# Kernel optimization log

Hardware: AMD Instinct MI355X
Metric: run time of the kernel (lower is better)

## Reference

```python
import jax, jax.numpy as jnp
import numpy as np

N_NODES = 100000
N_EDGES = 500000
N_GRAPHS = 128
HID = 128          # Config.hidden_dim
KEY_EMB = HID // 4 # 32
IN_DIM = 16
FEAT_DIM = IN_DIM - 1  # key feature removed
OUT_DIM = 2
MSG_IN = 2 * HID + 1   # 257


def setup_inputs() -> dict:
    key = jax.random.key(0)
    ks = jax.random.split(key, 24)
    p = lambda k, shp: (jax.random.normal(k, shp, dtype=jnp.float32) * 0.02)
    inp = {
        "x": jax.random.normal(ks[0], (N_NODES, IN_DIM), dtype=jnp.float32),
        "W_enc": p(ks[1], (1, KEY_EMB)), "b_enc": jnp.zeros((KEY_EMB,), jnp.float32),
        "W0": p(ks[2], (FEAT_DIM + KEY_EMB, HID)), "b0": jnp.zeros((HID,), jnp.float32),
        "W1a": p(ks[3], (MSG_IN, HID)), "b1a": jnp.zeros((HID,), jnp.float32),
        "W1b": p(ks[4], (HID, HID)), "b1b": jnp.zeros((HID,), jnp.float32),
        "W2a": p(ks[5], (MSG_IN, HID)), "b2a": jnp.zeros((HID,), jnp.float32),
        "W2b": p(ks[6], (HID, HID)), "b2b": jnp.zeros((HID,), jnp.float32),
        "Wf1": p(ks[7], (4 * HID, HID)), "bf1": jnp.zeros((HID,), jnp.float32),
        "Wf2": p(ks[8], (HID, OUT_DIM)), "bf2": jnp.zeros((OUT_DIM,), jnp.float32),
        "edge_src1": jax.random.randint(ks[9], (N_EDGES,), 0, N_NODES),
        "edge_dst1": jax.random.randint(ks[10], (N_EDGES,), 0, N_NODES),
        "edge_src2": jax.random.randint(ks[11], (N_EDGES,), 0, N_NODES),
        "edge_dst2": jax.random.randint(ks[12], (N_EDGES,), 0, N_NODES),
        "batch": jnp.sort(jax.random.randint(ks[13], (N_NODES,), 0, N_GRAPHS)),
    }
    return inp


def _leaky_relu(v):
    return jnp.where(v > 0, v, 0.1 * v)


def _edge_conv(h, key_feat, src, dst, Wa, ba, Wb, bb):
    # message: [x_j - x_i, x_i, key_j - key_i] -> Linear -> LeakyReLU(0.1) -> Linear
    h_i = h[dst]                      # [E, HID] target
    h_j = h[src]                      # [E, HID] source
    m = jnp.concatenate([h_j - h_i, h_i, key_feat[src] - key_feat[dst]], axis=-1)  # [E, 257]
    m = _leaky_relu(jnp.dot(m, Wa) + ba)
    m = jnp.dot(m, Wb) + bb
    agg = jax.ops.segment_max(m, dst, num_segments=N_NODES)
    agg = jnp.where(jnp.isfinite(agg), agg, 0.0)  # nodes with no in-edges -> 0 (PyG scatter-max fill)
    return agg + h  # residual


def reference(x, W_enc, b_enc, W0, b0, W1a, b1a, W1b, b1b, W2a, b2a, W2b, b2b,
              Wf1, bf1, Wf2, bf2, edge_src1, edge_dst1, edge_src2, edge_dst2, batch):
    key_feat = x[:, 0:1]              # key_feature_idx = 0
    features = x[:, 1:]               # [N, FEAT_DIM]
    key_emb = jnp.dot(key_feat, W_enc) + b_enc  # [N, 32]
    h = jax.nn.relu(jnp.dot(jnp.concatenate([features, key_emb], axis=-1), W0) + b0)  # dropout: eval mode

    x1 = jax.nn.relu(_edge_conv(h, key_feat, edge_src1, edge_dst1, W1a, b1a, W1b, b1b))
    x2 = jax.nn.relu(_edge_conv(x1, key_feat, edge_src2, edge_dst2, W2a, b2a, W2b, b2b))

    cat = jnp.concatenate([x1, x2], axis=1)  # [N, 256]
    max_pool = jax.ops.segment_max(cat, batch, num_segments=N_GRAPHS)
    max_pool = jnp.where(jnp.isfinite(max_pool), max_pool, 0.0)
    counts = jax.ops.segment_sum(jnp.ones((N_NODES,), jnp.float32), batch, num_segments=N_GRAPHS)
    mean_pool = jax.ops.segment_sum(cat, batch, num_segments=N_GRAPHS) / jnp.maximum(counts, 1.0)[:, None]

    pooled = jnp.concatenate([max_pool, mean_pool], axis=1)  # [G, 512]
    out = jnp.dot(jax.nn.relu(jnp.dot(pooled, Wf1) + bf1), Wf2) + bf2
    return jax.nn.log_softmax(out, axis=1)
```

## Files before the change

kernel.cpp:

```cpp
#include <hip/hip_runtime.h>
#include <cstdint>

#define N_NODES 100000
#define N_EDGES 500000
#define N_GRAPHS 128
#define HID 128
#define SCANH_B ((N_NODES + 255) / 256)
#define E256_G ((N_EDGES + 255) / 256)
#define MM_G ((N_NODES + 127) / 128)
#define AH_G ((N_NODES + 511) / 512)
#define BH_G ((N_EDGES + 511) / 512)
#define EDGE_G ((N_EDGES + 63) / 64)

typedef __attribute__((ext_vector_type(8))) short short8;
typedef __attribute__((ext_vector_type(4))) float f32x4;

__device__ __forceinline__ unsigned encf(float f) {
    unsigned u = __float_as_uint(f);
    return (u & 0x80000000u) ? ~u : (u | 0x80000000u);
}
__device__ __forceinline__ float decf(unsigned e) {
    unsigned u = (e & 0x80000000u) ? (e & 0x7FFFFFFFu) : ~e;
    return __uint_as_float(u);
}
__device__ __forceinline__ unsigned cvt_pk_bf16(float lo, float hi) {
    unsigned r;
    asm("v_cvt_pk_bf16_f32 %0, %1, %2" : "=v"(r) : "v"(lo), "v"(hi));
    return r;
}
__device__ __forceinline__ ushort bf16r(float f) {
    unsigned u = __float_as_uint(f);
    return (ushort)((u + 0x7fffu + ((u >> 16) & 1u)) >> 16);
}
__device__ __forceinline__ float bf2f(ushort h) {
    return __uint_as_float((unsigned)h << 16);
}

__global__ __launch_bounds__(256) void prep_hist_kernel(const float* __restrict__ W1b,
                                                        const float* __restrict__ W2b,
                                                        const float* __restrict__ W1a,
                                                        const float* __restrict__ W2a,
                                                        const float* __restrict__ W_enc,
                                                        const float* __restrict__ b_enc,
                                                        const float* __restrict__ W0,
                                                        const float* __restrict__ b0,
                                                        ushort* __restrict__ WT,
                                                        float* __restrict__ wkey,
                                                        float* __restrict__ bias0,
                                                        float* __restrict__ pooled,
                                                        const int* __restrict__ dst1,
                                                        int* __restrict__ cnt,
                                                        int* __restrict__ seq) {
    int blk = blockIdx.x;
    int tid = threadIdx.x;
    if (blk < E256_G) {
        int e = blk * 256 + tid;
        if (e < N_EDGES) seq[e] = atomicAdd(&cnt[dst1[e]], 1);
        return;
    }
    int b2 = blk - E256_G;
    if (b2 < 384) {
        int m = b2 >> 6;
        int i = (b2 & 63) * 256 + tid;
        int n = i >> 7, k = i & 127;
        int src = k * HID + n;
        float v;
        switch (m) {
            case 0: v = W1b[src]; break;
            case 1: v = W2b[src]; break;
            case 2: v = W1a[src]; break;
            case 3: v = W1a[HID * HID + src] - W1a[src]; break;
            case 4: v = W2a[src]; break;
            default: v = W2a[HID * HID + src] - W2a[src]; break;
        }
        WT[m * HID * HID + i] = bf16r(v);
        return;
    }
    if (b2 == 384) {
        if (tid < HID) {
            float wk = 0.f, bk = b0[tid];
            for (int k = 0; k < 32; ++k) {
                float w = W0[(15 + k) * HID + tid];
                wk += W_enc[k] * w;
                bk += b_enc[k] * w;
            }
            wkey[tid] = wk;
            bias0[tid] = bk;
        }
        return;
    }
    pooled[(b2 - 385) * 256 + tid] = 0.f;
}

__global__ __launch_bounds__(256) void scan_half_kernel(const int* __restrict__ cnt,
                                                        int* __restrict__ cursor,
                                                        int* __restrict__ partials) {
    __shared__ int tmp[256];
    int tid = threadIdx.x;
    int gid = blockIdx.x * 256 + tid;
    int v = (gid < N_NODES) ? cnt[gid] : 0;
    tmp[tid] = v;
    __syncthreads();
#pragma unroll
    for (int off = 1; off < 256; off <<= 1) {
        int t = (tid >= off) ? tmp[tid - off] : 0;
        __syncthreads();
        tmp[tid] += t;
        __syncthreads();
    }
    if (gid < N_NODES) cursor[gid] = tmp[tid] - v;
    if (tid == 255) partials[blockIdx.x] = tmp[255];
}

__global__ __launch_bounds__(512) void scan2_half_kernel(int* __restrict__ partials) {
    __shared__ int tmp[512];
    int tid = threadIdx.x;
    int v = (tid < SCANH_B) ? partials[tid] : 0;
    tmp[tid] = v;
    __syncthreads();
#pragma unroll
    for (int off = 1; off < 512; off <<= 1) {
        int t = (tid >= off) ? tmp[tid - off] : 0;
        __syncthreads();
        tmp[tid] += t;
        __syncthreads();
    }
    if (tid < SCANH_B) partials[tid] = tmp[tid] - v;
}

__global__ __launch_bounds__(512, 4) void build_mm_kernel(const float* __restrict__ x,
                                                          const float* __restrict__ W0,
                                                          const float* __restrict__ wkey,
                                                          const float* __restrict__ bias0,
                                                          ushort* __restrict__ h,
                                                          float* __restrict__ xkey,
                                                          const ushort* __restrict__ WuT,
                                                          const ushort* __restrict__ WvT,
                                                          const float* __restrict__ bv,
                                                          ushort* __restrict__ outu,
                                                          ushort* __restrict__ outv,
                                                          const int* __restrict__ src1,
                                                          const int* __restrict__ dst1,
                                                          const int* __restrict__ cnt,
                                                          const int* __restrict__ cursor,
                                                          const int* __restrict__ partials1,
                                                          const int* __restrict__ seq,
                                                          int* __restrict__ srcS,
                                                          int* __restrict__ dstS,
                                                          unsigned* __restrict__ agg1) {
    __shared__ ushort sH[128 * 136];
    __shared__ ushort sWT[128 * 136];
    int blk = blockIdx.x;
    int tid = threadIdx.x;

    if (blk >= MM_G) {
        int zb = blk - MM_G;
        if (zb < AH_G) {
            int gid = zb * 512 + tid;
            if (gid >= N_NODES) return;
            int c = cnt[gid];
            if (c == 0) return;
            int o = cursor[gid] + partials1[gid >> 8];
            for (int i = 0; i < c; ++i) dstS[o + i] = gid;
            bool spans = (o >> 4) != ((o + c - 1) >> 4);
            bool tail = (o + c == N_EDGES);
            if (spans || tail) {
                uint4* ap = (uint4*)(agg1 + (size_t)gid * HID);
#pragma unroll
                for (int i = 0; i < 32; ++i) ap[i] = make_uint4(0u, 0u, 0u, 0u);
            }
            return;
        }
        {
            int e = (zb - AH_G) * 512 + tid;
            if (e >= N_EDGES) return;
            int idx = dst1[e];
            int pos = cursor[idx] + partials1[idx >> 8] + seq[e];
            srcS[pos] = src1[e];
            return;
        }
    }

    int n0 = blk * 128;
#pragma unroll
    for (int q = 0; q < 4; ++q) {
        int c = q * 512 + tid;
        int r = c >> 4, off = (c & 15) << 3;
        int n = n0 + r;
        uint4 vv = make_uint4(0, 0, 0, 0);
        if (n < N_NODES) {
            const float* xr = x + n * 16;
            float k0 = xr[0];
            if (off == 0) xkey[n] = k0;
            float xf[15];
#pragma unroll
            for (int f = 0; f < 15; ++f) xf[f] = xr[1 + f];
            unsigned ow[4];
#pragma unroll
            for (int p = 0; p < 4; ++p) {
                int c0 = off + 2 * p;
                float a0 = bias0[c0] + k0 * wkey[c0];
                float a1 = bias0[c0 + 1] + k0 * wkey[c0 + 1];
#pragma unroll
                for (int f = 0; f < 15; ++f) {
                    float2 w2 = *(const float2*)(W0 + f * HID + c0);
                    a0 = fmaf(xf[f], w2.x, a0);
                    a1 = fmaf(xf[f], w2.y, a1);
                }
                ow[p] = cvt_pk_bf16(fmaxf(a0, 0.f), fmaxf(a1, 0.f));
            }
            vv = make_uint4(ow[0], ow[1], ow[2], ow[3]);
            *(uint4*)(h + (size_t)n * HID + off) = vv;
        }
        *(uint4*)(sH + r * 136 + off) = vv;
    }
#pragma unroll
    for (int q = 0; q < 4; ++q) {
        int c = q * 512 + tid;
        int nn = c >> 4, off = (c & 15) << 3;
        *(uint4*)(sWT + nn * 136 + off) = *(const uint4*)(WuT + nn * 128 + off);
    }
    __syncthreads();

    int lane = tid & 63, wv = tid >> 6;
    int l15 = lane & 15, quad = lane >> 4;
    int ch = wv & 1, rh = wv >> 1;

    short8 afr[2][4];
#pragma unroll
    for (int rr = 0; rr < 2; ++rr) {
        const ushort* ab = sH + (rh * 32 + rr * 16 + l15) * 136 + quad * 8;
#pragma unroll
        for (int kc = 0; kc < 4; ++kc)
            afr[rr][kc] = *(const short8*)(ab + kc * 32);
    }

#pragma unroll
    for (int pass = 0; pass < 2; ++pass) {
        ushort* out = pass ? outv : outu;
        f32x4 acc[2][4];
#pragma unroll
        for (int rr = 0; rr < 2; ++rr)
#pragma unroll
            for (int ct = 0; ct < 4; ++ct) acc[rr][ct] = (f32x4){0.f, 0.f, 0.f, 0.f};
#pragma unroll
        for (int kc = 0; kc < 4; ++kc) {
#pragma unroll
            for (int ct = 0; ct < 4; ++ct) {
                short8 bfr = *(const short8*)(sWT + ((ch * 4 + ct) * 16 + l15) * 136 + quad * 8 + kc * 32);
                acc[0][ct] = __builtin_amdgcn_mfma_f32_16x16x32_bf16(afr[0][kc], bfr, acc[0][ct], 0, 0, 0);
                acc[1][ct] = __builtin_amdgcn_mfma_f32_16x16x32_bf16(afr[1][kc], bfr, acc[1][ct], 0, 0, 0);
            }
        }
        __syncthreads();
#pragma unroll
        for (int ct = 0; ct < 4; ++ct) {
            int col = (ch * 4 + ct) * 16 + l15;
            float bb = pass ? bv[col] : 0.f;
#pragma unroll
            for (int rr = 0; rr < 2; ++rr) {
                int rowb = rh * 32 + rr * 16 + quad * 4;
                unsigned p01 = cvt_pk_bf16(acc[rr][ct][0] + bb, acc[rr][ct][1] + bb);
                unsigned p23 = cvt_pk_bf16(acc[rr][ct][2] + bb, acc[rr][ct][3] + bb);
                sH[(rowb + 0) * 136 + col] = (ushort)p01;
                sH[(rowb + 1) * 136 + col] = (ushort)(p01 >> 16);
                sH[(rowb + 2) * 136 + col] = (ushort)p23;
                sH[(rowb + 3) * 136 + col] = (ushort)(p23 >> 16);
            }
        }
        if (pass == 0) {
#pragma unroll
            for (int q = 0; q < 4; ++q) {
                int c = q * 512 + tid;
                int nn = c >> 4, off = (c & 15) << 3;
                *(uint4*)(sWT + nn * 136 + off) = *(const uint4*)(WvT + nn * 128 + off);
            }
        }
        __syncthreads();
#pragma unroll
        for (int q = 0; q < 4; ++q) {
            int c = q * 512 + tid;
            int r = c >> 4, off = (c & 15) << 3;
            int m = n0 + r;
            if (m < N_NODES)
                *(uint4*)(out + (size_t)m * HID + off) = *(const uint4*)(sH + r * 136 + off);
        }
    }
}

__global__ __launch_bounds__(512, 4) void mm2_build2_kernel(const ushort* __restrict__ in,
                                                            const unsigned* __restrict__ aggin,
                                                            const int* __restrict__ cntin,
                                                            const float* __restrict__ baddin,
                                                            ushort* __restrict__ xout,
                                                            const ushort* __restrict__ WuT,
                                                            const ushort* __restrict__ WvT,
                                                            const float* __restrict__ bv,
                                                            ushort* __restrict__ outu,
                                                            ushort* __restrict__ outv,
                                                            const int* __restrict__ src2,
                                                            const int* __restrict__ dst2,
                                                            const int* __restrict__ cnt2,
                                                            const int* __restrict__ cursor2,
                                                            const int* __restrict__ partials2,
                                                            const int* __restrict__ seq,
                                                            int* __restrict__ srcS,
                                                            int* __restrict__ dstS,
                                                            unsigned* __restrict__ agg2) {
    __shared__ ushort sH[128 * 136];
    __shared__ ushort sWT[128 * 136];
    int blk = blockIdx.x;
    int tid = threadIdx.x;

    if (blk < BH_G) {
        int e = blk * 512 + tid;
        if (e >= N_EDGES) return;
        int idx = dst2[e];
        int pos = cursor2[idx] + partials2[idx >> 8] + seq[N_EDGES + e];
        srcS[N_EDGES + pos] = src2[e];
        return;
    }
    int b = blk - BH_G;
    if (b < AH_G) {
        int gid = b * 512 + tid;
        if (gid >= N_NODES) return;
        int c = cnt2[gid];
        if (c == 0) return;
        int o = cursor2[gid] + partials2[gid >> 8];
        for (int i = 0; i < c; ++i) dstS[N_EDGES + o + i] = gid;
        bool spans = (o >> 4) != ((o + c - 1) >> 4);
        bool tail = (o + c == N_EDGES);
        if (spans || tail) {
            uint4* ap = (uint4*)(agg2 + (size_t)gid * HID);
#pragma unroll
            for (int i = 0; i < 32; ++i) ap[i] = make_uint4(0u, 0u, 0u, 0u);
        }
        return;
    }

    int n0 = (b - AH_G) * 128;
#pragma unroll
    for (int q = 0; q < 4; ++q) {
        int c = q * 512 + tid;
        int r = c >> 4, off = (c & 15) << 3;
        int n = n0 + r;
        uint4 vv = make_uint4(0, 0, 0, 0);
        if (n < N_NODES) {
            uint4 hv = *(const uint4*)(in + (size_t)n * HID + off);
            float add[8];
#pragma unroll
            for (int p = 0; p < 8; ++p) add[p] = 0.f;
            if (cntin[n] > 0) {
                uint4 e0 = *(const uint4*)(aggin + (size_t)n * HID + off);
                uint4 e1 = *(const uint4*)(aggin + (size_t)n * HID + off + 4);
                float4 bb0 = *(const float4*)(baddin + off);
                float4 bb1 = *(const float4*)(baddin + off + 4);
                add[0] = decf(e0.x) + bb0.x; add[1] = decf(e0.y) + bb0.y;
                add[2] = decf(e0.z) + bb0.z; add[3] = decf(e0.w) + bb0.w;
                add[4] = decf(e1.x) + bb1.x; add[5] = decf(e1.y) + bb1.y;
                add[6] = decf(e1.z) + bb1.z; add[7] = decf(e1.w) + bb1.w;
            }
            unsigned hw[4] = {hv.x, hv.y, hv.z, hv.w};
            unsigned ow[4];
#pragma unroll
            for (int p = 0; p < 4; ++p) {
                float lo = __uint_as_float(hw[p] << 16);
                float hi = __uint_as_float(hw[p] & 0xffff0000u);
                float r0 = fmaxf(add[2 * p] + lo, 0.f);
                float r1 = fmaxf(add[2 * p + 1] + hi, 0.f);
                ow[p] = cvt_pk_bf16(r0, r1);
            }
            vv = make_uint4(ow[0], ow[1], ow[2], ow[3]);
            *(uint4*)(xout + (size_t)n * HID + off) = vv;
        }
        *(uint4*)(sH + r * 136 + off) = vv;
    }
#pragma unroll
    for (int q = 0; q < 4; ++q) {
        int c = q * 512 + tid;
        int nn = c >> 4, off = (c & 15) << 3;
        *(uint4*)(sWT + nn * 136 + off) = *(const uint4*)(WuT + nn * 128 + off);
    }
    __syncthreads();

    int lane = tid & 63, wv = tid >> 6;
    int l15 = lane & 15, quad = lane >> 4;
    int ch = wv & 1, rh = wv >> 1;

    short8 afr[2][4];
#pragma unroll
    for (int rr = 0; rr < 2; ++rr) {
        const ushort* ab = sH + (rh * 32 + rr * 16 + l15) * 136 + quad * 8;
#pragma unroll
        for (int kc = 0; kc < 4; ++kc)
            afr[rr][kc] = *(const short8*)(ab + kc * 32);
    }

#pragma unroll
    for (int pass = 0; pass < 2; ++pass) {
        ushort* out = pass ? outv : outu;
        f32x4 acc[2][4];
#pragma unroll
        for (int rr = 0; rr < 2; ++rr)
#pragma unroll
            for (int ct = 0; ct < 4; ++ct) acc[rr][ct] = (f32x4){0.f, 0.f, 0.f, 0.f};
#pragma unroll
        for (int kc = 0; kc < 4; ++kc) {
#pragma unroll
            for (int ct = 0; ct < 4; ++ct) {
                short8 bfr = *(const short8*)(sWT + ((ch * 4 + ct) * 16 + l15) * 136 + quad * 8 + kc * 32);
                acc[0][ct] = __builtin_amdgcn_mfma_f32_16x16x32_bf16(afr[0][kc], bfr, acc[0][ct], 0, 0, 0);
                acc[1][ct] = __builtin_amdgcn_mfma_f32_16x16x32_bf16(afr[1][kc], bfr, acc[1][ct], 0, 0, 0);
            }
        }
        __syncthreads();
#pragma unroll
        for (int ct = 0; ct < 4; ++ct) {
            int col = (ch * 4 + ct) * 16 + l15;
            float bb = pass ? bv[col] : 0.f;
#pragma unroll
            for (int rr = 0; rr < 2; ++rr) {
                int rowb = rh * 32 + rr * 16 + quad * 4;
                unsigned p01 = cvt_pk_bf16(acc[rr][ct][0] + bb, acc[rr][ct][1] + bb);
                unsigned p23 = cvt_pk_bf16(acc[rr][ct][2] + bb, acc[rr][ct][3] + bb);
                sH[(rowb + 0) * 136 + col] = (ushort)p01;
                sH[(rowb + 1) * 136 + col] = (ushort)(p01 >> 16);
                sH[(rowb + 2) * 136 + col] = (ushort)p23;
                sH[(rowb + 3) * 136 + col] = (ushort)(p23 >> 16);
            }
        }
        if (pass == 0) {
#pragma unroll
            for (int q = 0; q < 4; ++q) {
                int c = q * 512 + tid;
                int nn = c >> 4, off = (c & 15) << 3;
                *(uint4*)(sWT + nn * 136 + off) = *(const uint4*)(WvT + nn * 128 + off);
            }
        }
        __syncthreads();
#pragma unroll
        for (int q = 0; q < 4; ++q) {
            int c = q * 512 + tid;
            int r = c >> 4, off = (c & 15) << 3;
            int m = n0 + r;
            if (m < N_NODES)
                *(uint4*)(out + (size_t)m * HID + off) = *(const uint4*)(sH + r * 136 + off);
        }
    }
}

__global__ __launch_bounds__(512, 6) void edge_kernel(const ushort* __restrict__ u,
                                                      const ushort* __restrict__ v,
                                                      const float* __restrict__ xkey,
                                                      const int* __restrict__ srcS,
                                                      const int* __restrict__ dstS,
                                                      const ushort* __restrict__ WbT,
                                                      const float* __restrict__ wlast,
                                                      unsigned* __restrict__ agg,
                                                      const int* __restrict__ dst2h,
                                                      int* __restrict__ cnt2w,
                                                      int* __restrict__ seqh,
                                                      int histN) {
    __shared__ ushort sWT[128 * 136];
    __shared__ ushort sU[64 * 136];
    __shared__ int sDst[64];
    __shared__ int sBnd[2];
    __shared__ unsigned sMask[3];
    int tid = threadIdx.x;

    int wg;
    if (histN) {
        int r9 = blockIdx.x % 9, q9 = blockIdx.x / 9;
        if (r9 == 0) {
            int e = q9 * 512 + tid;
            if (e < N_EDGES) seqh[e] = atomicAdd(&cnt2w[dst2h[e]], 1);
            return;
        }
        wg = q9 * 8 + (r9 - 1);
        if (wg >= EDGE_G) return;
    } else {
        wg = blockIdx.x;
    }

    const int nwg = EDGE_G;
    int qq = nwg >> 3, rr8 = nwg & 7;
    int xcd = wg & 7, idx = wg >> 3;
    int wgid = (xcd < rr8 ? xcd * (qq + 1) : rr8 * (qq + 1) + (xcd - rr8) * qq) + idx;
    int w0 = wgid * 64;

#pragma unroll
    for (int q = 0; q < 4; ++q) {
        int c = q * 512 + tid;
        int n = c >> 4, off = (c & 15) << 3;
        *(uint4*)(sWT + n * 136 + off) = *(const uint4*)(WbT + n * 128 + off);
    }

    int eloc = tid >> 3;
    int sub = tid & 7;
    int kb = sub << 4;
    int lane = tid & 63, wv = tid >> 6;
    int l15 = lane & 15, quad = lane >> 4;
    int ch = wv & 1, rh = wv >> 1;

    float wreg[16];
    {
        const float4* wr4 = (const float4*)(wlast + kb);
#pragma unroll
        for (int q = 0; q < 4; ++q) {
            float4 wq = wr4[q];
            wreg[q * 4 + 0] = wq.x; wreg[q * 4 + 1] = wq.y;
            wreg[q * 4 + 2] = wq.z; wreg[q * 4 + 3] = wq.w;
        }
    }

    {
        int e = w0 + eloc;
        if (e >= N_EDGES) e = N_EDGES - 1;
        int sx = srcS[e], sy = dstS[e];
        if (sub == 0) sDst[eloc] = sy;
        if (tid < 2) {
            int eb = (tid == 0) ? (w0 - 1) : (w0 + 64);
            sBnd[tid] = (eb >= 0 && eb < N_EDGES) ? dstS[eb] : -1;
        }
        float kd = xkey[sx] - xkey[sy];
        const uint4* ur = (const uint4*)(u + (size_t)sx * HID + kb);
        const uint4* vr = (const uint4*)(v + (size_t)sy * HID + kb);
        uint4 uu[2], vvv[2];
        uu[0] = ur[0]; uu[1] = ur[1];
        vvv[0] = vr[0]; vvv[1] = vr[1];
#pragma unroll
        for (int q = 0; q < 2; ++q) {
            unsigned pu[4] = {uu[q].x, uu[q].y, uu[q].z, uu[q].w};
            unsigned pv[4] = {vvv[q].x, vvv[q].y, vvv[q].z, vvv[q].w};
            unsigned pk[4];
#pragma unroll
            for (int p = 0; p < 4; ++p) {
                float a0 = __uint_as_float(pu[p] << 16) + __uint_as_float(pv[p] << 16);
                float a1 = __uint_as_float(pu[p] & 0xffff0000u) + __uint_as_float(pv[p] & 0xffff0000u);
                a0 = fmaf(kd, wreg[q * 8 + 2 * p], a0);
                a1 = fmaf(kd, wreg[q * 8 + 2 * p + 1], a1);
                a0 = fmaxf(a0, 0.1f * a0);
                a1 = fmaxf(a1, 0.1f * a1);
                pk[p] = cvt_pk_bf16(a0, a1);
            }
            uint4 o; o.x = pk[0]; o.y = pk[1]; o.z = pk[2]; o.w = pk[3];
            *(uint4*)(sU + eloc * 136 + kb + q * 8) = o;
        }
    }
    __syncthreads();

    if (tid < 64) {
        int dprev = (tid == 0) ? sBnd[0] : sDst[tid - 1];
        unsigned long long m = __ballot(sDst[tid] != dprev);
        if (tid == 0) { sMask[0] = (unsigned)m; sMask[1] = (unsigned)(m >> 32); }
        if (tid == 63) sMask[2] = (sDst[63] != sBnd[1]) ? 1u : 0u;
    }

    short8 afr[4];
    {
        const ushort* ab = sU + (rh * 16 + l15) * 136 + quad * 8;
#pragma unroll
        for (int kc = 0; kc < 4; ++kc)
            afr[kc] = *(const short8*)(ab + kc * 32);
    }
    f32x4 acc[4];
#pragma unroll
    for (int ct = 0; ct < 4; ++ct) acc[ct] = (f32x4){0.f, 0.f, 0.f, 0.f};
#pragma unroll
    for (int kc = 0; kc < 4; ++kc) {
#pragma unroll
        for (int ct = 0; ct < 4; ++ct) {
            short8 bfr = *(const short8*)(sWT + ((ch * 4 + ct) * 16 + l15) * 136 + quad * 8 + kc * 32);
            acc[ct] = __builtin_amdgcn_mfma_f32_16x16x32_bf16(afr[kc], bfr, acc[ct], 0, 0, 0);
        }
    }
    __syncthreads();

#pragma unroll
    for (int ct = 0; ct < 4; ++ct) {
        int col = (ch * 4 + ct) * 16 + l15;
        uint2 pr;
        pr.x = cvt_pk_bf16(acc[ct][0], acc[ct][1]);
        pr.y = cvt_pk_bf16(acc[ct][2], acc[ct][3]);
        *(uint2*)(sU + col * 66 + rh * 16 + quad * 4) = pr;
    }
    __syncthreads();

    {
        int j = tid & 127;
        int q4 = tid >> 7;
        int base = q4 * 16;
        const ushort* mrow = sU + j * 66 + base;
        float vals[16];
#pragma unroll
        for (int q = 0; q < 4; ++q) {
            ushort4 mv = *(const ushort4*)(mrow + q * 4);
            vals[q * 4 + 0] = bf2f(mv.x);
            vals[q * 4 + 1] = bf2f(mv.y);
            vals[q * 4 + 2] = bf2f(mv.z);
            vals[q * 4 + 3] = bf2f(mv.w);
        }
        unsigned mlo = __builtin_amdgcn_readfirstlane(sMask[0]);
        unsigned mhi = __builtin_amdgcn_readfirstlane(sMask[1]);
        unsigned b64 = __builtin_amdgcn_readfirstlane(sMask[2]);
        unsigned long long mask = ((unsigned long long)mhi << 32) | mlo;
        unsigned slice = (unsigned)((mask >> base) & 0xFFFFull);
        unsigned nextbit = (q4 == 3) ? (b64 & 1u) : (unsigned)((mask >> (base + 16)) & 1ull);
        unsigned ext = slice | (nextbit << 16);
        bool contFrom = !(ext & 1u);
        float run = 0.f;
        bool first = true;
#pragma unroll
        for (int e3 = 0; e3 < 16; ++e3) {
            float vv2 = vals[e3];
            bool hb = (ext >> e3) & 1u;
            run = (e3 == 0 || hb) ? vv2 : fmaxf(run, vv2);
            bool end = (e3 == 15) || ((ext >> (e3 + 1)) & 1u);
            if (end) {
                int d = sDst[base + e3];
                unsigned en = encf(run);
                unsigned* ap = agg + (size_t)d * HID + j;
                bool useAtomic = (first && contFrom) || ((e3 == 15) && !nextbit);
                if (useAtomic) atomicMax(ap, en);
                else *ap = en;
                first = false;
            }
        }
    }
}

__global__ __launch_bounds__(256) void pool_kernel(const ushort* __restrict__ x1,
                                                   const unsigned* __restrict__ agg2,
                                                   const float* __restrict__ b2b,
                                                   const int* __restrict__ cnt2,
                                                   const int* __restrict__ batch,
                                                   float* __restrict__ pooled) {
    int g = blockIdx.x >> 4, s = blockIdx.x & 15;
    int tid = threadIdx.x;
    int lo = 0, hi = N_NODES;
    while (lo < hi) { int mid = (lo + hi) >> 1; if (batch[mid] < g) lo = mid + 1; else hi = mid; }
    int start = lo;
    hi = N_NODES;
    while (lo < hi) { int mid = (lo + hi) >> 1; if (batch[mid] < g + 1) lo = mid + 1; else hi = mid; }
    int end = lo;
    int cnt = end - start;
    int b0 = start + (int)((long long)cnt * s / 16);
    int b1 = start + (int)((long long)cnt * (s + 1) / 16);
    if (b1 <= b0) return;
    int j = tid & 127;
    bool isx2 = tid >= 128;
    float bbj = isx2 ? b2b[j] : 0.f;
    float mx = -INFINITY, sm = 0.f;
    for (int n = b0; n < b1; ++n) {
        float xv = bf2f(x1[(size_t)n * HID + j]);
        float vv;
        if (isx2) {
            float a = 0.f;
            if (cnt2[n] > 0) a = decf(agg2[(size_t)n * HID + j]) + bbj;
            vv = fmaxf(a + xv, 0.f);
        } else {
            vv = xv;
        }
        mx = fmaxf(mx, vv);
        sm += vv;
    }
    atomicMax((unsigned*)pooled + (size_t)g * 512 + tid, encf(mx));
    atomicAdd(pooled + (size_t)g * 512 + 256 + tid, sm);
}

__global__ __launch_bounds__(128) void final_kernel(const float* __restrict__ pooled,
                                                    const int* __restrict__ batch,
                                                    const float* __restrict__ Wf1,
                                                    const float* __restrict__ bf1,
                                                    const float* __restrict__ Wf2,
                                                    const float* __restrict__ bf2,
                                                    float* __restrict__ out) {
    __shared__ float sP[512];
    __shared__ float sH[128];
    int g = blockIdx.x, tid = threadIdx.x;
    int lo = 0, hi = N_NODES;
    while (lo < hi) { int mid = (lo + hi) >> 1; if (batch[mid] < g) lo = mid + 1; else hi = mid; }
    int start = lo;
    hi = N_NODES;
    while (lo < hi) { int mid = (lo + hi) >> 1; if (batch[mid] < g + 1) lo = mid + 1; else hi = mid; }
    int cnt = lo - start;
    float inv = 1.f / (float)(cnt > 1 ? cnt : 1);
#pragma unroll
    for (int q = 0; q < 4; ++q) {
        int idx = q * 128 + tid;
        float raw;
        if (idx < 256) {
            unsigned e = ((const unsigned*)pooled)[(size_t)g * 512 + idx];
            raw = (e == 0u) ? 0.f : decf(e);
        } else {
            raw = pooled[(size_t)g * 512 + idx] * inv;
        }
        sP[idx] = raw;
    }
    __syncthreads();
    float acc = bf1[tid];
    for (int k = 0; k < 512; ++k) acc = fmaf(sP[k], Wf1[k * HID + tid], acc);
    sH[tid] = fmaxf(acc, 0.f);
    __syncthreads();
    if (tid < 2) {
        float l = bf2[tid];
        for (int k = 0; k < 128; ++k) l = fmaf(sH[k], Wf2[k * 2 + tid], l);
        sP[tid] = l;
    }
    __syncthreads();
    if (tid == 0) {
        float l0 = sP[0], l1 = sP[1];
        float m = fmaxf(l0, l1);
        float ls = m + logf(expf(l0 - m) + expf(l1 - m));
        out[g * 2 + 0] = l0 - ls;
        out[g * 2 + 1] = l1 - ls;
    }
}

extern "C" void kernel_launch(void* const* d_in, const int* in_sizes, int n_in,
                              void* d_out, int out_size, void* d_ws, size_t ws_size,
                              hipStream_t stream) {
    const float* x     = (const float*)d_in[0];
    const float* W_enc = (const float*)d_in[1];
    const float* b_enc = (const float*)d_in[2];
    const float* W0    = (const float*)d_in[3];
    const float* b0    = (const float*)d_in[4];
    const float* W1a   = (const float*)d_in[5];
    const float* b1a   = (const float*)d_in[6];
    const float* W1b   = (const float*)d_in[7];
    const float* b1b   = (const float*)d_in[8];
    const float* W2a   = (const float*)d_in[9];
    const float* b2a   = (const float*)d_in[10];
    const float* W2b   = (const float*)d_in[11];
    const float* b2b   = (const float*)d_in[12];
    const float* Wf1   = (const float*)d_in[13];
    const float* bf1   = (const float*)d_in[14];
    const float* Wf2   = (const float*)d_in[15];
    const float* bf2   = (const float*)d_in[16];
    const int* src1    = (const int*)d_in[17];
    const int* dst1    = (const int*)d_in[18];
    const int* src2    = (const int*)d_in[19];
    const int* dst2    = (const int*)d_in[20];
    const int* batch   = (const int*)d_in[21];

    const size_t NB = (size_t)N_NODES * HID;
    ushort* hbuf  = (ushort*)d_ws;
    unsigned* agg1 = (unsigned*)(hbuf + NB);
    unsigned* agg2 = agg1 + NB;
    ushort* ubuf  = (ushort*)(agg2 + NB);
    ushort* vbuf  = ubuf + NB;
    ushort* WT    = vbuf + NB;
    ushort* WbT1 = WT;
    ushort* WbT2 = WT + 1 * HID * HID;
    ushort* WuT1 = WT + 2 * HID * HID;
    ushort* WvT1 = WT + 3 * HID * HID;
    ushort* WuT2 = WT + 4 * HID * HID;
    ushort* WvT2 = WT + 5 * HID * HID;
    float* wkey  = (float*)(WT + 6 * HID * HID);
    float* bias0 = wkey + 128;
    float* xkey  = bias0 + 128;
    float* pooled = xkey + N_NODES;
    int* cnt    = (int*)(pooled + 128 * 512);
    int* cursor = cnt + 2 * N_NODES;
    int* partials1 = cursor + 2 * N_NODES;
    int* partials2 = partials1 + 512;
    int* srcS = partials2 + 512;
    int* dstS = srcS + 2 * N_EDGES;
    int* seq  = dstS + 2 * N_EDGES;

    const int prepGrid = E256_G + 385 + 256;
    const int buildMmGrid = MM_G + AH_G + BH_G;
    const int mm2Grid = BH_G + AH_G + MM_G;
    const int edge1Grid = EDGE_G + BH_G;

    hipMemsetAsync(cnt, 0, 2 * N_NODES * sizeof(int), stream);
    prep_hist_kernel<<<prepGrid, 256, 0, stream>>>(W1b, W2b, W1a, W2a, W_enc, b_enc, W0, b0,
                                                   WT, wkey, bias0, pooled, dst1, cnt, seq);
    scan_half_kernel<<<SCANH_B, 256, 0, stream>>>(cnt, cursor, partials1);
    scan2_half_kernel<<<1, 512, 0, stream>>>(partials1);

    build_mm_kernel<<<buildMmGrid, 512, 0, stream>>>(x, W0, wkey, bias0, hbuf, xkey,
                                                     WuT1, WvT1, b1a, ubuf, vbuf,
                                                     src1, dst1, cnt, cursor, partials1,
                                                     seq, srcS, dstS, agg1);

    edge_kernel<<<edge1Grid, 512, 0, stream>>>(ubuf, vbuf, xkey, srcS, dstS, WbT1,
                                               W1a + 256 * HID, agg1,
                                               dst2, cnt + N_NODES, seq + N_EDGES, 1);

    scan_half_kernel<<<SCANH_B, 256, 0, stream>>>(cnt + N_NODES, cursor + N_NODES, partials2);
    scan2_half_kernel<<<1, 512, 0, stream>>>(partials2);

    mm2_build2_kernel<<<mm2Grid, 512, 0, stream>>>(hbuf, agg1, cnt, b1b, hbuf,
                                                   WuT2, WvT2, b2a, ubuf, vbuf,
                                                   src2, dst2, cnt + N_NODES, cursor + N_NODES,
                                                   partials2, seq, srcS, dstS, agg2);
    edge_kernel<<<EDGE_G, 512, 0, stream>>>(ubuf, vbuf, xkey, srcS + N_EDGES, dstS + N_EDGES,
                                            WbT2, W2a + 256 * HID, agg2,
                                            nullptr, nullptr, nullptr, 0);

    pool_kernel<<<N_GRAPHS * 16, 256, 0, stream>>>(hbuf, agg2, b2b, cnt + N_NODES, batch, pooled);
    final_kernel<<<N_GRAPHS, 128, 0, stream>>>(pooled, batch, Wf1, bf1, Wf2, bf2, (float*)d_out);
}
```

Before: 439.2 us.

## Fold edge histogram and CSR build work into matmul blocks

The layer-1 destination histogram (atomic counting) moves from the prep kernel into the node-matmul kernel. Each matmul block handles 640 edges and writes seq only at the end, so the atomic latency overlaps the GEMM. The layer-1 CSR scatter becomes its own kernel that runs after the scan. The layer-2 scatter and dstS fill are spread across the matmul blocks instead of living in separate extra blocks. __syncthreads is replaced with a raw lgkmcnt wait plus s_barrier. The goal is fewer lightweight blocks and more latency hiding, but it adds one kernel launch and makes the matmul blocks heavier.

New measurement: 451.3 us. +2.8%, slower.

```diff
diff --git a/kernel.cpp b/kernel.cpp
--- a/kernel.cpp
+++ b/kernel.cpp
@@ -6,14 +6,18 @@
 #define N_GRAPHS 128
 #define HID 128
 #define SCANH_B ((N_NODES + 255) / 256)
-#define E256_G ((N_EDGES + 255) / 256)
 #define MM_G ((N_NODES + 127) / 128)
 #define AH_G ((N_NODES + 511) / 512)
 #define BH_G ((N_EDGES + 511) / 512)
 #define EDGE_G ((N_EDGES + 63) / 64)
+#define EPB 640
 
 typedef __attribute__((ext_vector_type(8))) short short8;
 typedef __attribute__((ext_vector_type(4))) float f32x4;
+
+__device__ __forceinline__ void wg_barrier() {
+    asm volatile("s_waitcnt lgkmcnt(0)\n\ts_barrier" ::: "memory");
+}
 
 __device__ __forceinline__ unsigned encf(float f) {
     unsigned u = __float_as_uint(f);
@@ -36,32 +40,23 @@
     return __uint_as_float((unsigned)h << 16);
 }
 
-__global__ __launch_bounds__(256) void prep_hist_kernel(const float* __restrict__ W1b,
-                                                        const float* __restrict__ W2b,
-                                                        const float* __restrict__ W1a,
-                                                        const float* __restrict__ W2a,
-                                                        const float* __restrict__ W_enc,
-                                                        const float* __restrict__ b_enc,
-                                                        const float* __restrict__ W0,
-                                                        const float* __restrict__ b0,
-                                                        ushort* __restrict__ WT,
-                                                        float* __restrict__ wkey,
-                                                        float* __restrict__ bias0,
-                                                        float* __restrict__ pooled,
-                                                        const int* __restrict__ dst1,
-                                                        int* __restrict__ cnt,
-                                                        int* __restrict__ seq) {
+__global__ __launch_bounds__(256) void prep_kernel(const float* __restrict__ W1b,
+                                                   const float* __restrict__ W2b,
+                                                   const float* __restrict__ W1a,
+                                                   const float* __restrict__ W2a,
+                                                   const float* __restrict__ W_enc,
+                                                   const float* __restrict__ b_enc,
+                                                   const float* __restrict__ W0,
+                                                   const float* __restrict__ b0,
+                                                   ushort* __restrict__ WT,
+                                                   float* __restrict__ wkey,
+                                                   float* __restrict__ bias0,
+                                                   float* __restrict__ pooled) {
     int blk = blockIdx.x;
     int tid = threadIdx.x;
-    if (blk < E256_G) {
-        int e = blk * 256 + tid;
-        if (e < N_EDGES) seq[e] = atomicAdd(&cnt[dst1[e]], 1);
-        return;
-    }
-    int b2 = blk - E256_G;
-    if (b2 < 384) {
-        int m = b2 >> 6;
-        int i = (b2 & 63) * 256 + tid;
+    if (blk < 384) {
+        int m = blk >> 6;
+        int i = (blk & 63) * 256 + tid;
         int n = i >> 7, k = i & 127;
         int src = k * HID + n;
         float v;
@@ -76,7 +71,7 @@
         WT[m * HID * HID + i] = bf16r(v);
         return;
     }
-    if (b2 == 384) {
+    if (blk == 384) {
         if (tid < HID) {
             float wk = 0.f, bk = b0[tid];
             for (int k = 0; k < 32; ++k) {
@@ -89,7 +84,7 @@
         }
         return;
     }
-    pooled[(b2 - 385) * 256 + tid] = 0.f;
+    pooled[(blk - 385) * 256 + tid] = 0.f;
 }
 
 __global__ __launch_bounds__(256) void scan_half_kernel(const int* __restrict__ cnt,
@@ -128,58 +123,30 @@
     if (tid < SCANH_B) partials[tid] = tmp[tid] - v;
 }
 
-__global__ __launch_bounds__(512, 4) void build_mm_kernel(const float* __restrict__ x,
-                                                          const float* __restrict__ W0,
-                                                          const float* __restrict__ wkey,
-                                                          const float* __restrict__ bias0,
-                                                          ushort* __restrict__ h,
-                                                          float* __restrict__ xkey,
-                                                          const ushort* __restrict__ WuT,
-                                                          const ushort* __restrict__ WvT,
-                                                          const float* __restrict__ bv,
-                                                          ushort* __restrict__ outu,
-                                                          ushort* __restrict__ outv,
-                                                          const int* __restrict__ src1,
-                                                          const int* __restrict__ dst1,
-                                                          const int* __restrict__ cnt,
-                                                          const int* __restrict__ cursor,
-                                                          const int* __restrict__ partials1,
-                                                          const int* __restrict__ seq,
-                                                          int* __restrict__ srcS,
-                                                          int* __restrict__ dstS,
-                                                          unsigned* __restrict__ agg1) {
+__global__ __launch_bounds__(512, 4) void mm1_hist1_kernel(const float* __restrict__ x,
+                                                           const float* __restrict__ W0,
+                                                           const float* __restrict__ wkey,
+                                                           const float* __restrict__ bias0,
+                                                           ushort* __restrict__ h,
+                                                           float* __restrict__ xkey,
+                                                           const ushort* __restrict__ WuT,
+                                                           const ushort* __restrict__ WvT,
+                                                           const float* __restrict__ bv,
+                                                           ushort* __restrict__ outu,
+                                                           ushort* __restrict__ outv,
+                                                           const int* __restrict__ dst1,
+                                                           int* __restrict__ cnt,
+                                                           int* __restrict__ seq) {
     __shared__ ushort sH[128 * 136];
     __shared__ ushort sWT[128 * 136];
     int blk = blockIdx.x;
     int tid = threadIdx.x;
 
-    if (blk >= MM_G) {
-        int zb = blk - MM_G;
-        if (zb < AH_G) {
-            int gid = zb * 512 + tid;
-            if (gid >= N_NODES) return;
-            int c = cnt[gid];
-            if (c == 0) return;
-            int o = cursor[gid] + partials1[gid >> 8];
-            for (int i = 0; i < c; ++i) dstS[o + i] = gid;
-            bool spans = (o >> 4) != ((o + c - 1) >> 4);
-            bool tail = (o + c == N_EDGES);
-            if (spans || tail) {
-                uint4* ap = (uint4*)(agg1 + (size_t)gid * HID);
-#pragma unroll
-                for (int i = 0; i < 32; ++i) ap[i] = make_uint4(0u, 0u, 0u, 0u);
-            }
-            return;
-        }
-        {
-            int e = (zb - AH_G) * 512 + tid;
-            if (e >= N_EDGES) return;
-            int idx = dst1[e];
-            int pos = cursor[idx] + partials1[idx >> 8] + seq[e];
-            srcS[pos] = src1[e];
-            return;
-        }
-    }
+    int he0 = blk * EPB + tid;
+    int he1 = he0 + 512;
+    int rv0 = 0, rv1 = 0;
+    if (he0 < N_EDGES) rv0 = atomicAdd(&cnt[dst1[he0]], 1);
+    if (tid < EPB - 512 && he1 < N_EDGES) rv1 = atomicAdd(&cnt[dst1[he1]], 1);
 
     int n0 = blk * 128;
 #pragma unroll
@@ -220,7 +187,7 @@
         int nn = c >> 4, off = (c & 15) << 3;
         *(uint4*)(sWT + nn * 136 + off) = *(const uint4*)(WuT + nn * 128 + off);
     }
-    __syncthreads();
+    wg_barrier();
 
     int lane = tid & 63, wv = tid >> 6;
     int l15 = lane & 15, quad = lane >> 4;
@@ -252,7 +219,7 @@
                 acc[1][ct] = __builtin_amdgcn_mfma_f32_16x16x32_bf16(afr[1][kc], bfr, acc[1][ct], 0, 0, 0);
             }
         }
-        __syncthreads();
+        wg_barrier();
 #pragma unroll
         for (int ct = 0; ct < 4; ++ct) {
             int col = (ch * 4 + ct) * 16 + l15;
@@ -276,7 +243,7 @@
                 *(uint4*)(sWT + nn * 136 + off) = *(const uint4*)(WvT + nn * 128 + off);
             }
         }
-        __syncthreads();
+        wg_barrier();
 #pragma unroll
         for (int q = 0; q < 4; ++q) {
             int c = q * 512 + tid;
@@ -286,59 +253,104 @@
                 *(uint4*)(out + (size_t)m * HID + off) = *(const uint4*)(sH + r * 136 + off);
         }
     }
-}
-
-__global__ __launch_bounds__(512, 4) void mm2_build2_kernel(const ushort* __restrict__ in,
-                                                            const unsigned* __restrict__ aggin,
-                                                            const int* __restrict__ cntin,
-                                                            const float* __restrict__ baddin,
-                                                            ushort* __restrict__ xout,
-                                                            const ushort* __restrict__ WuT,
-                                                            const ushort* __restrict__ WvT,
-                                                            const float* __restrict__ bv,
-                                                            ushort* __restrict__ outu,
-                                                            ushort* __restrict__ outv,
-                                                            const int* __restrict__ src2,
-                                                            const int* __restrict__ dst2,
-                                                            const int* __restrict__ cnt2,
-                                                            const int* __restrict__ cursor2,
-                                                            const int* __restrict__ partials2,
-                                                            const int* __restrict__ seq,
-                                                            int* __restrict__ srcS,
-                                                            int* __restrict__ dstS,
-                                                            unsigned* __restrict__ agg2) {
+
+    if (he0 < N_EDGES) seq[he0] = rv0;
+    if (tid < EPB - 512 && he1 < N_EDGES) seq[he1] = rv1;
+}
+
+__global__ __launch_bounds__(512) void build1_kernel(const int* __restrict__ src1,
+                                                     const int* __restrict__ dst1,
+                                                     const int* __restrict__ cnt,
+                                                     const int* __restrict__ cursor,
+                                                     const int* __restrict__ partials1,
+                                                     const int* __restrict__ seq,
+                                                     int* __restrict__ srcS,
+                                                     int* __restrict__ dstS,
+                                                     unsigned* __restrict__ agg1) {
+    int blk = blockIdx.x;
+    int tid = threadIdx.x;
+    if (blk < AH_G) {
+        int gid = blk * 512 + tid;
+        if (gid >= N_NODES) return;
+        int c = cnt[gid];
+        if (c == 0) return;
+        int o = cursor[gid] + partials1[gid >> 8];
+        for (int i = 0; i < c; ++i) dstS[o + i] = gid;
+        bool spans = (o >> 4) != ((o + c - 1) >> 4);
+        bool tail = (o + c == N_EDGES);
+        if (spans || tail) {
+            uint4* ap = (uint4*)(agg1 + (size_t)gid * HID);
+#pragma unroll
+            for (int i = 0; i < 32; ++i) ap[i] = make_uint4(0u, 0u, 0u, 0u);
+        }
+        return;
+    }
+    int e = (blk - AH_G) * 512 + tid;
+    if (e >= N_EDGES) return;
+    int idx = dst1[e];
+    int pos = cursor[idx] + partials1[idx >> 8] + seq[e];
+    srcS[pos] = src1[e];
+}
+
+__global__ __launch_bounds__(512, 4) void mm2_fused_kernel(const ushort* __restrict__ in,
+                                                           const unsigned* __restrict__ aggin,
+                                                           const int* __restrict__ cntin,
+                                                           const float* __restrict__ baddin,
+                                                           ushort* __restrict__ xout,
+                                                           const ushort* __restrict__ WuT,
+                                                           const ushort* __restrict__ WvT,
+                                                           const float* __restrict__ bv,
+                                                           ushort* __restrict__ outu,
+                                                           ushort* __restrict__ outv,
+                                                           const int* __restrict__ src2,
+                                                           const int* __restrict__ dst2,
+                                                           const int* __restrict__ cnt2,
+                                                           const int* __restrict__ cursor2,
+                                                           const int* __restrict__ partials2,
+                                                           const int* __restrict__ seq,
+                                                           int* __restrict__ srcS,
+                                                           int* __restrict__ dstS,
+                                                           unsigned* __restrict__ agg2) {
     __shared__ ushort sH[128 * 136];
     __shared__ ushort sWT[128 * 136];
     int blk = blockIdx.x;
     int tid = threadIdx.x;
-
-    if (blk < BH_G) {
-        int e = blk * 512 + tid;
-        if (e >= N_EDGES) return;
-        int idx = dst2[e];
-        int pos = cursor2[idx] + partials2[idx >> 8] + seq[N_EDGES + e];
-        srcS[N_EDGES + pos] = src2[e];
-        return;
-    }
-    int b = blk - BH_G;
-    if (b < AH_G) {
-        int gid = b * 512 + tid;
-        if (gid >= N_NODES) return;
-        int c = cnt2[gid];
-        if (c == 0) return;
-        int o = cursor2[gid] + partials2[gid >> 8];
-        for (int i = 0; i < c; ++i) dstS[N_EDGES + o + i] = gid;
-        bool spans = (o >> 4) != ((o + c - 1) >> 4);
-        bool tail = (o + c == N_EDGES);
-        if (spans || tail) {
-            uint4* ap = (uint4*)(agg2 + (size_t)gid * HID);
-#pragma unroll
-            for (int i = 0; i < 32; ++i) ap[i] = make_uint4(0u, 0u, 0u, 0u);
-        }
-        return;
-    }
-
-    int n0 = (b - AH_G) * 128;
+    int n0 = blk * 128;
+
+    {
+        int e0 = blk * EPB + tid;
+        if (e0 < N_EDGES) {
+            int idx = dst2[e0];
+            int pos = cursor2[idx] + partials2[idx >> 8] + seq[N_EDGES + e0];
+            srcS[N_EDGES + pos] = src2[e0];
+        }
+        if (tid < EPB - 512) {
+            int e1 = e0 + 512;
+            if (e1 < N_EDGES) {
+                int idx = dst2[e1];
+                int pos = cursor2[idx] + partials2[idx >> 8] + seq[N_EDGES + e1];
+                srcS[N_EDGES + pos] = src2[e1];
+            }
+        }
+    }
+    if (tid < 128) {
+        int gid = n0 + tid;
+        if (gid < N_NODES) {
+            int c = cnt2[gid];
+            if (c) {
+                int o = cursor2[gid] + partials2[gid >> 8];
+                for (int i = 0; i < c; ++i) dstS[N_EDGES + o + i] = gid;
+                bool spans = (o >> 4) != ((o + c - 1) >> 4);
+                bool tail = (o + c == N_EDGES);
+                if (spans || tail) {
+                    uint4* ap = (uint4*)(agg2 + (size_t)gid * HID);
+#pragma unroll
+                    for (int i = 0; i < 32; ++i) ap[i] = make_uint4(0u, 0u, 0u, 0u);
+                }
+            }
+        }
+    }
+
 #pragma unroll
     for (int q = 0; q < 4; ++q) {
         int c = q * 512 + tid;
@@ -381,7 +393,7 @@
         int nn = c >> 4, off = (c & 15) << 3;
         *(uint4*)(sWT + nn * 136 + off) = *(const uint4*)(WuT + nn * 128 + off);
     }
-    __syncthreads();
+    wg_barrier();
 
     int lane = tid & 63, wv = tid >> 6;
     int l15 = lane & 15, quad = lane >> 4;
@@ -413,7 +425,7 @@
                 acc[1][ct] = __builtin_amdgcn_mfma_f32_16x16x32_bf16(afr[1][kc], bfr, acc[1][ct], 0, 0, 0);
             }
         }
-        __syncthreads();
+        wg_barrier();
 #pragma unroll
         for (int ct = 0; ct < 4; ++ct) {
             int col = (ch * 4 + ct) * 16 + l15;
@@ -437,7 +449,7 @@
                 *(uint4*)(sWT + nn * 136 + off) = *(const uint4*)(WvT + nn * 128 + off);
             }
         }
-        __syncthreads();
+        wg_barrier();
 #pragma unroll
         for (int q = 0; q < 4; ++q) {
             int c = q * 512 + tid;
@@ -768,21 +780,22 @@
     int* dstS = srcS + 2 * N_EDGES;
     int* seq  = dstS + 2 * N_EDGES;
 
-    const int prepGrid = E256_G + 385 + 256;
-    const int buildMmGrid = MM_G + AH_G + BH_G;
-    const int mm2Grid = BH_G + AH_G + MM_G;
+    const int prepGrid = 385 + 256;
+    const int build1Grid = AH_G + BH_G;
     const int edge1Grid = EDGE_G + BH_G;
 
     hipMemsetAsync(cnt, 0, 2 * N_NODES * sizeof(int), stream);
-    prep_hist_kernel<<<prepGrid, 256, 0, stream>>>(W1b, W2b, W1a, W2a, W_enc, b_enc, W0, b0,
-                                                   WT, wkey, bias0, pooled, dst1, cnt, seq);
+    prep_kernel<<<prepGrid, 256, 0, stream>>>(W1b, W2b, W1a, W2a, W_enc, b_enc, W0, b0,
+                                              WT, wkey, bias0, pooled);
+
+    mm1_hist1_kernel<<<MM_G, 512, 0, stream>>>(x, W0, wkey, bias0, hbuf, xkey,
+                                               WuT1, WvT1, b1a, ubuf, vbuf,
+                                               dst1, cnt, seq);
     scan_half_kernel<<<SCANH_B, 256, 0, stream>>>(cnt, cursor, partials1);
     scan2_half_kernel<<<1, 512, 0, stream>>>(partials1);
 
-    build_mm_kernel<<<buildMmGrid, 512, 0, stream>>>(x, W0, wkey, bias0, hbuf, xkey,
-                                                     WuT1, WvT1, b1a, ubuf, vbuf,
-                                                     src1, dst1, cnt, cursor, partials1,
-                                                     seq, srcS, dstS, agg1);
+    build1_kernel<<<build1Grid, 512, 0, stream>>>(src1, dst1, cnt, cursor, partials1,
+                                                  seq, srcS, dstS, agg1);
 
     edge_kernel<<<edge1Grid, 512, 0, stream>>>(ubuf, vbuf, xkey, srcS, dstS, WbT1,
                                                W1a + 256 * HID, agg1,
@@ -791,10 +804,10 @@
     scan_half_kernel<<<SCANH_B, 256, 0, stream>>>(cnt + N_NODES, cursor + N_NODES, partials2);
     scan2_half_kernel<<<1, 512, 0, stream>>>(partials2);
 
-    mm2_build2_kernel<<<mm2Grid, 512, 0, stream>>>(hbuf, agg1, cnt, b1b, hbuf,
-                                                   WuT2, WvT2, b2a, ubuf, vbuf,
-                                                   src2, dst2, cnt + N_NODES, cursor + N_NODES,
-                                                   partials2, seq, srcS, dstS, agg2);
+    mm2_fused_kernel<<<MM_G, 512, 0, stream>>>(hbuf, agg1, cnt, b1b, hbuf,
+                                               WuT2, WvT2, b2a, ubuf, vbuf,
+                                               src2, dst2, cnt + N_NODES, cursor + N_NODES,
+                                               partials2, seq, srcS, dstS, agg2);
     edge_kernel<<<EDGE_G, 512, 0, stream>>>(ubuf, vbuf, xkey, srcS + N_EDGES, dstS + N_EDGES,
                                             WbT2, W2a + 256 * HID, agg2,
                                             nullptr, nullptr, nullptr, 0);
```
